# Performance work log

Measured on AMD Instinct MI355X. Metric: run time of the kernel, lower is better.

The kernel has to match this reference:

```python
import jax, jax.numpy as jnp
import numpy as np

BATCH, L, DM, DS, K, EXPAND = 4, 2048, 1024, 16, 4, 2
DI = EXPAND * DM  # 2048


def setup_inputs() -> dict:
    key = jax.random.key(0)
    ks = jax.random.split(key, 12)
    s = 0.02  # small init so exp(exp(dt)*A) and tanh stay well-behaved
    return {
        "x": jax.random.normal(ks[0], (BATCH, L, DM), jnp.float32),
        "W_in": jax.random.normal(ks[1], (2 * DI, DM), jnp.float32) * s,
        "b_in": jax.random.normal(ks[2], (2 * DI,), jnp.float32) * s,
        "conv_w": jax.random.normal(ks[3], (DI, 1, K), jnp.float32) * s,  # depthwise
        "conv_b": jax.random.normal(ks[4], (DI,), jnp.float32) * s,
        "W_x": jax.random.normal(ks[5], (2 * DS, DI), jnp.float32) * s,
        "b_x": jax.random.normal(ks[6], (2 * DS,), jnp.float32) * s,
        "dt": jax.random.normal(ks[7], (DI,), jnp.float32) * s,
        "A": jax.random.normal(ks[8], (DS, DS), jnp.float32) * s,
        "D": jnp.ones((DI,), jnp.float32),
        "W_out": jax.random.normal(ks[9], (DM, DI), jnp.float32) * s,
        "b_out": jax.random.normal(ks[10], (DM,), jnp.float32) * s,
    }


def _forward(x, W_in, b_in, conv_w, conv_b, W_x, b_x, dt, A, D, W_out, b_out):
    # in_proj: (B, L, 2*DI), split into conv path and residual
    xr = x @ W_in.T + b_in
    xi, res = jnp.split(xr, 2, axis=-1)
    # depthwise causal conv1d: torch pads both sides by K-1 then truncates to L,
    # equivalent to left-pad-only causal conv
    xc = jax.lax.conv_general_dilated(
        xi.transpose(0, 2, 1), conv_w, window_strides=(1,),
        padding=((K - 1, 0),), feature_group_count=DI,
        dimension_numbers=("NCH", "OIH", "NCH"))
    xc = (xc + conv_b[None, :, None]).transpose(0, 2, 1)  # (B, L, DI)
    xs = jax.nn.silu(xc)
    # x_proj -> B, C (each (B, L, DS))
    bc = xs @ W_x.T + b_x
    Bm, Cm = jnp.split(bc, 2, axis=-1)
    # dt = exp(self.dt) sliced to first DS entries, indexed per step by i % DS
    dtv = jnp.exp(dt)[:DS]
    dt_seq = dtv[jnp.arange(L) % DS]  # (L,)
    # NOTE: torch code computes x * D inside _selective_scan but never uses it;
    # the scan output depends only on dt, A, B, C.

    def step(h, inp):
        d_i, B_t, C_t = inp  # scalar, (B, DS), (B, DS)
        A_t = jnp.exp(d_i * A)  # (DS, DS)
        h_new = jnp.tanh(jnp.einsum("ij,bj->bi", A_t, h) + B_t * h + C_t)
        return h_new, h_new

    h0 = jnp.zeros((x.shape[0], DS), x.dtype)
    _, hs = jax.lax.scan(step, h0, (dt_seq, Bm.transpose(1, 0, 2), Cm.transpose(1, 0, 2)))
    hs = hs.transpose(1, 0, 2)  # (B, L, DS)
    y = jnp.tile(hs, (1, 1, DI // DS)) + res  # repeat state to d_inner, add res
    return y @ W_out.T + b_out


def reference(x, W_in, b_in, conv_w, conv_b, W_x, b_x, dt, A, D, W_out, b_out):
    return _forward(x, W_in, b_in, conv_w, conv_b, W_x, b_x, dt, A, D, W_out, b_out)
```

## Files before the change

### kernel.cpp

```cpp
#include <hip/hip_runtime.h>
#include <cstdint>
#include <cstddef>

typedef __attribute__((ext_vector_type(4))) float f32x4;
typedef __attribute__((ext_vector_type(8))) __bf16 bf16x8;
typedef __attribute__((ext_vector_type(4))) unsigned int u32x4;
typedef __attribute__((ext_vector_type(2))) unsigned int u32x2;

#define DEVFN static __device__ __forceinline__

#define OFF_XBF    0ull
#define OFF_WINBF  16777216ull
#define OFF_WXBF   25165824ull
#define OFF_WOUTBF 25296896ull
#define OFF_WRED   29491200ull
#define OFF_XIBF   29556736ull
#define OFF_RESBF  63111168ull
#define OFF_XSBF   96665600ull
#define OFF_BC     130220032ull
#define OFF_HS     131268608ull

DEVFN unsigned short f2bf(float f) {
  unsigned u = __float_as_uint(f);
  return (unsigned short)((u + 0x7FFFu + ((u >> 16) & 1u)) >> 16);
}

DEVFN void gload_lds16(const void* g, void* l) {
  __builtin_amdgcn_global_load_lds(
      (const __attribute__((address_space(1))) void*)g,
      (__attribute__((address_space(3))) void*)l, 16, 0, 0);
}

#define DPPF(x, ctrl) \
  __int_as_float(__builtin_amdgcn_update_dpp(0, __float_as_int(x), ctrl, 0xF, 0xF, true))

DEVFN void cvt8(const float* __restrict__ in, unsigned short* __restrict__ out, int t) {
  f32x4 a = *(const f32x4*)(in + (size_t)t * 8);
  f32x4 b = *(const f32x4*)(in + (size_t)t * 8 + 4);
  u32x4 r;
  r.x = (unsigned)f2bf(a[0]) | ((unsigned)f2bf(a[1]) << 16);
  r.y = (unsigned)f2bf(a[2]) | ((unsigned)f2bf(a[3]) << 16);
  r.z = (unsigned)f2bf(b[0]) | ((unsigned)f2bf(b[1]) << 16);
  r.w = (unsigned)f2bf(b[2]) | ((unsigned)f2bf(b[3]) << 16);
  *(u32x4*)(out + (size_t)t * 8) = r;
}

__global__ __launch_bounds__(256) void k_prep(
    const float* __restrict__ x, const float* __restrict__ W_in,
    const float* __restrict__ W_x, const float* __restrict__ W_out,
    unsigned short* __restrict__ xbf, unsigned short* __restrict__ winbf,
    unsigned short* __restrict__ wxbf, unsigned short* __restrict__ woutbf,
    float* __restrict__ wred) {
  const int bid = blockIdx.x, tid = threadIdx.x;
  if (bid < 4096)      cvt8(x,     xbf,    bid * 256 + tid);
  else if (bid < 6144) cvt8(W_in,  winbf,  (bid - 4096) * 256 + tid);
  else if (bid < 6176) cvt8(W_x,   wxbf,   (bid - 6144) * 256 + tid);
  else if (bid < 7200) cvt8(W_out, woutbf, (bid - 6176) * 256 + tid);
  else {
    const int t = (bid - 7200) * 256 + tid;
    const int m = t >> 4, j = t & 15;
    float s = 0.f;
    for (int r = 0; r < 128; r++) s += W_out[(size_t)m * 2048 + r * 16 + j];
    wred[t] = s;
  }
}

template <int EPI>
DEVFN void gemm128(const unsigned short* __restrict__ Ag,
                   const unsigned short* __restrict__ Bg, int K,
                   int m0, int n0, const float* __restrict__ bias,
                   float* __restrict__ outf,
                   unsigned short* __restrict__ ob0,
                   unsigned short* __restrict__ ob1) {
  __shared__ unsigned short As[128 * 64];
  __shared__ unsigned short Bs[128 * 64];
  const int tid = threadIdx.x;
  const int wave = tid >> 6, lane = tid & 63;
  const int wm = wave >> 1, wn = wave & 1;
  const int fr = lane & 15;
  const int k8 = (lane >> 4) << 3;

  f32x4 acc[4][4];
#pragma unroll
  for (int a = 0; a < 4; a++)
#pragma unroll
    for (int b = 0; b < 4; b++) acc[a][b] = f32x4{0.f, 0.f, 0.f, 0.f};

  for (int kt = 0; kt < K; kt += 64) {
#pragma unroll
    for (int i = 0; i < 4; i++) {
      const int base = (wave << 10) + (i << 12);
      const int off = base + (lane << 4);
      const int row = off >> 7;
      const int col = (off & 127) >> 1;
      gload_lds16(Ag + (size_t)(m0 + row) * K + kt + col, (char*)As + base);
      gload_lds16(Bg + (size_t)(n0 + row) * K + kt + col, (char*)Bs + base);
    }
    __syncthreads();
#pragma unroll
    for (int kk = 0; kk < 2; kk++) {
      bf16x8 af[4], bfr[4];
#pragma unroll
      for (int f = 0; f < 4; f++) {
        af[f]  = *(const bf16x8*)&As[(wm * 64 + f * 16 + fr) * 64 + kk * 32 + k8];
        bfr[f] = *(const bf16x8*)&Bs[(wn * 64 + f * 16 + fr) * 64 + kk * 32 + k8];
      }
#pragma unroll
      for (int fi = 0; fi < 4; fi++)
#pragma unroll
        for (int fj = 0; fj < 4; fj++)
          acc[fi][fj] = __builtin_amdgcn_mfma_f32_16x16x32_bf16(
              af[fi], bfr[fj], acc[fi][fj], 0, 0, 0);
    }
    __syncthreads();
  }

  const int r0 = (lane >> 4) * 4;
#pragma unroll
  for (int fj = 0; fj < 4; fj++) {
    const int col = n0 + wn * 64 + fj * 16 + fr;
    const float bia = (EPI == 0) ? bias[col] : 0.f;
#pragma unroll
    for (int fi = 0; fi < 4; fi++) {
      const int rowb = m0 + wm * 64 + fi * 16 + r0;
#pragma unroll
      for (int r = 0; r < 4; r++) {
        const float v = acc[fi][fj][r] + bia;
        if (EPI == 0) {
          if (col < 2048) ob0[(size_t)(rowb + r) * 2048 + col] = f2bf(v);
          else            ob1[(size_t)(rowb + r) * 2048 + (col - 2048)] = f2bf(v);
        } else {
          outf[(size_t)(rowb + r) * 1024 + col] = v;
        }
      }
    }
  }
}

__global__ __launch_bounds__(256) void k_gemm1(const unsigned short* __restrict__ xbf,
                                               const unsigned short* __restrict__ winbf,
                                               const float* __restrict__ b_in,
                                               unsigned short* __restrict__ xibf,
                                               unsigned short* __restrict__ resbf) {
  const int bid = blockIdx.x;
  gemm128<0>(xbf, winbf, 1024, (bid >> 5) * 128, (bid & 31) * 128, b_in,
             nullptr, xibf, resbf);
}

__global__ __launch_bounds__(256) void k_conv(const unsigned short* __restrict__ xi,
                                              const float* __restrict__ cw,
                                              const float* __restrict__ cb,
                                              unsigned short* __restrict__ xs) {
  const int t = blockIdx.x * 256 + threadIdx.x;
  const int c4 = t & 511;
  const int lc = (t >> 9) & 255;
  const int b  = t >> 17;
  const int l0 = lc * 8;
  const int c0 = c4 * 4;
  const unsigned short* xb = xi + ((size_t)(b * 2048 + l0)) * 2048 + c0;
  u32x2 raw[11];
#pragma unroll
  for (int j = 0; j < 11; j++) {
    const int l = l0 + j - 3;
    raw[j] = (l >= 0) ? *(const u32x2*)(xb + ((long)j - 3) * 2048) : u32x2{0u, 0u};
  }
  f32x4 val[11];
#pragma unroll
  for (int j = 0; j < 11; j++) {
    val[j][0] = __uint_as_float(raw[j].x << 16);
    val[j][1] = __uint_as_float(raw[j].x & 0xFFFF0000u);
    val[j][2] = __uint_as_float(raw[j].y << 16);
    val[j][3] = __uint_as_float(raw[j].y & 0xFFFF0000u);
  }
  const f32x4 w0 = *(const f32x4*)(cw + (size_t)c0 * 4);
  const f32x4 w1 = *(const f32x4*)(cw + (size_t)(c0 + 1) * 4);
  const f32x4 w2 = *(const f32x4*)(cw + (size_t)(c0 + 2) * 4);
  const f32x4 w3 = *(const f32x4*)(cw + (size_t)(c0 + 3) * 4);
  const f32x4 bb = *(const f32x4*)(cb + c0);
  unsigned short* xp = xs + ((size_t)(b * 2048 + l0)) * 2048 + c0;
#pragma unroll
  for (int jo = 0; jo < 8; jo++) {
    f32x4 v;
    v[0] = bb[0] + w0[0]*val[jo][0] + w0[1]*val[jo+1][0] + w0[2]*val[jo+2][0] + w0[3]*val[jo+3][0];
    v[1] = bb[1] + w1[0]*val[jo][1] + w1[1]*val[jo+1][1] + w1[2]*val[jo+2][1] + w1[3]*val[jo+3][1];
    v[2] = bb[2] + w2[0]*val[jo][2] + w2[1]*val[jo+1][2] + w2[2]*val[jo+2][2] + w2[3]*val[jo+3][2];
    v[3] = bb[3] + w3[0]*val[jo][3] + w3[1]*val[jo+1][3] + w3[2]*val[jo+2][3] + w3[3]*val[jo+3][3];
#pragma unroll
    for (int q = 0; q < 4; q++) {
      const float x = v[q];
      v[q] = x * __builtin_amdgcn_rcpf(1.f + __expf(-x));
    }
    u32x2 rr;
    rr.x = (unsigned)f2bf(v[0]) | ((unsigned)f2bf(v[1]) << 16);
    rr.y = (unsigned)f2bf(v[2]) | ((unsigned)f2bf(v[3]) << 16);
    *(u32x2*)(xp + (size_t)jo * 2048) = rr;
  }
}

__global__ __launch_bounds__(256) void k_gemm2(const unsigned short* __restrict__ xs,
                                               const unsigned short* __restrict__ wx,
                                               const float* __restrict__ bx,
                                               float* __restrict__ bc) {
  __shared__ unsigned short As[128 * 64];
  __shared__ unsigned short Bs[32 * 64];
  const int tid = threadIdx.x, wave = tid >> 6, lane = tid & 63;
  const int m0 = blockIdx.x * 128;
  const int fr = lane & 15, k8 = (lane >> 4) << 3;
  f32x4 acc[2][2];
#pragma unroll
  for (int a = 0; a < 2; a++)
#pragma unroll
    for (int b = 0; b < 2; b++) acc[a][b] = f32x4{0.f, 0.f, 0.f, 0.f};

  for (int kt = 0; kt < 2048; kt += 64) {
#pragma unroll
    for (int i = 0; i < 4; i++) {
      const int base = (wave << 10) + (i << 12);
      const int off = base + (lane << 4);
      const int row = off >> 7, col = (off & 127) >> 1;
      gload_lds16(xs + (size_t)(m0 + row) * 2048 + kt + col, (char*)As + base);
    }
    {
      const int base = (wave << 10);
      const int off = base + (lane << 4);
      const int row = off >> 7, col = (off & 127) >> 1;
      gload_lds16(wx + (size_t)row * 2048 + kt + col, (char*)Bs + base);
    }
    __syncthreads();
#pragma unroll
    for (int kk = 0; kk < 2; kk++) {
      bf16x8 af[2], bfr[2];
#pragma unroll
      for (int f = 0; f < 2; f++) {
        af[f]  = *(const bf16x8*)&As[(wave * 32 + f * 16 + fr) * 64 + kk * 32 + k8];
        bfr[f] = *(const bf16x8*)&Bs[(f * 16 + fr) * 64 + kk * 32 + k8];
      }
#pragma unroll
      for (int fi = 0; fi < 2; fi++)
#pragma unroll
        for (int fj = 0; fj < 2; fj++)
          acc[fi][fj] = __builtin_amdgcn_mfma_f32_16x16x32_bf16(
              af[fi], bfr[fj], acc[fi][fj], 0, 0, 0);
    }
    __syncthreads();
  }
  const int r0 = (lane >> 4) * 4;
#pragma unroll
  for (int fi = 0; fi < 2; fi++)
#pragma unroll
    for (int fj = 0; fj < 2; fj++) {
      const int col = fj * 16 + fr;
      const float bia = bx[col];
#pragma unroll
      for (int r = 0; r < 4; r++) {
        const int row = m0 + wave * 32 + fi * 16 + r0 + r;
        bc[(size_t)row * 32 + col] = acc[fi][fj][r] + bia;
      }
    }
}

DEVFN float scan4_step(float h, const f32x4 ax, float Bt, float Ct, int a0) {
  const int hv = __float_as_int(h);
  const float g0 = __int_as_float(__builtin_amdgcn_ds_bpermute(a0,      hv));
  const float g1 = __int_as_float(__builtin_amdgcn_ds_bpermute(a0 + 16, hv));
  const float g2 = __int_as_float(__builtin_amdgcn_ds_bpermute(a0 + 32, hv));
  const float g3 = __int_as_float(__builtin_amdgcn_ds_bpermute(a0 + 48, hv));
  const float pa = fmaf(ax[1], g1, ax[0] * g0);
  const float pb = fmaf(ax[3], g3, ax[2] * g2);
  float p = pa + pb;
  p += DPPF(p, 0xB1);
  p += DPPF(p, 0x4E);
  const float s = p + fmaf(Bt, h, Ct);
  const float e = __expf(2.f * s);
  return fmaf(-2.f, __builtin_amdgcn_rcpf(e + 1.f), 1.f);
}

__global__ __launch_bounds__(256) void k4_gemm3_scan(
    const unsigned short* __restrict__ resbf, const unsigned short* __restrict__ woutbf,
    float* __restrict__ out, const float* __restrict__ bc, const float* __restrict__ dt,
    const float* __restrict__ Amat, float* __restrict__ hs) {
  if (blockIdx.x < 512) {
    const int bid = blockIdx.x;
    gemm128<1>(resbf, woutbf, 2048, (bid >> 3) * 128, (bid & 7) * 128, nullptr,
               out, nullptr, nullptr);
    return;
  }
  const int tid = threadIdx.x;
  const int b = tid >> 6;
  const int lane = tid & 63;
  const int i = lane >> 2, k = lane & 3;

  const f32x4 arow = *(const f32x4*)(Amat + i * 16 + k * 4);
  f32x4 axv[16];
#pragma unroll
  for (int p = 0; p < 16; p++) {
    const float e = __expf(dt[p]);
    axv[p][0] = __expf(e * arow[0]);
    axv[p][1] = __expf(e * arow[1]);
    axv[p][2] = __expf(e * arow[2]);
    axv[p][3] = __expf(e * arow[3]);
  }
  const int a0 = (lane & 3) << 6;
  const float* bcp = bc + (size_t)b * 65536 + i;
  float* hsp = hs + (size_t)b * 32768 + i;
  float h = 0.f;

  float p0B[8], p0C[8], p1B[8], p1C[8];
#pragma unroll
  for (int q = 0; q < 8; q++) { p0B[q] = bcp[q * 32]; p0C[q] = bcp[q * 32 + 16]; }

  for (int l0 = 0; l0 < 2048; l0 += 16) {
    {
      const float* bq = bcp + (size_t)(l0 + 8) * 32;
#pragma unroll
      for (int q = 0; q < 8; q++) { p1B[q] = bq[q * 32]; p1C[q] = bq[q * 32 + 16]; }
    }
#pragma unroll
    for (int q = 0; q < 8; q++) {
      h = scan4_step(h, axv[q], p0B[q], p0C[q], a0);
      if (k == 0) hsp[(size_t)(l0 + q) * 16] = h;
    }
    {
      const float* bq = bcp + (size_t)((l0 + 16) & 2047) * 32;
#pragma unroll
      for (int q = 0; q < 8; q++) { p0B[q] = bq[q * 32]; p0C[q] = bq[q * 32 + 16]; }
    }
#pragma unroll
    for (int q = 8; q < 16; q++) {
      h = scan4_step(h, axv[q], p1B[q - 8], p1C[q - 8], a0);
      if (k == 0) hsp[(size_t)(l0 + q) * 16] = h;
    }
  }
}

__global__ __launch_bounds__(256) void k5_combine(float* __restrict__ out,
                                                  const float* __restrict__ hs,
                                                  const float* __restrict__ wred,
                                                  const float* __restrict__ bo) {
  const int m4 = threadIdx.x;
  const int rg = blockIdx.x;
  f32x4 w[4][4];
#pragma unroll
  for (int mi = 0; mi < 4; mi++)
#pragma unroll
    for (int q = 0; q < 4; q++)
      w[mi][q] = *(const f32x4*)&wred[(size_t)(m4 * 4 + mi) * 16 + q * 4];
  const f32x4 bov = *(const f32x4*)&bo[m4 * 4];
#pragma unroll
  for (int r = 0; r < 4; r++) {
    const size_t row = (size_t)rg * 4 + r;
    f32x4 hv[4];
#pragma unroll
    for (int q = 0; q < 4; q++) hv[q] = *(const f32x4*)&hs[row * 16 + q * 4];
    float* op = out + row * 1024 + m4 * 4;
    f32x4 o = *(f32x4*)op;
#pragma unroll
    for (int mi = 0; mi < 4; mi++) {
      float v = bov[mi];
#pragma unroll
      for (int q = 0; q < 4; q++)
        v += w[mi][q][0]*hv[q][0] + w[mi][q][1]*hv[q][1] +
             w[mi][q][2]*hv[q][2] + w[mi][q][3]*hv[q][3];
      o[mi] += v;
    }
    *(f32x4*)op = o;
  }
}

extern "C" void kernel_launch(void* const* d_in, const int* in_sizes, int n_in,
                              void* d_out, int out_size, void* d_ws, size_t ws_size,
                              hipStream_t stream) {
  const float* x      = (const float*)d_in[0];
  const float* W_in   = (const float*)d_in[1];
  const float* b_in   = (const float*)d_in[2];
  const float* conv_w = (const float*)d_in[3];
  const float* conv_b = (const float*)d_in[4];
  const float* W_x    = (const float*)d_in[5];
  const float* b_x    = (const float*)d_in[6];
  const float* dt     = (const float*)d_in[7];
  const float* A      = (const float*)d_in[8];
  const float* W_out  = (const float*)d_in[10];
  const float* b_out  = (const float*)d_in[11];
  float* out = (float*)d_out;

  char* ws = (char*)d_ws;
  unsigned short* xbf    = (unsigned short*)(ws + OFF_XBF);
  unsigned short* winbf  = (unsigned short*)(ws + OFF_WINBF);
  unsigned short* wxbf   = (unsigned short*)(ws + OFF_WXBF);
  unsigned short* woutbf = (unsigned short*)(ws + OFF_WOUTBF);
  float*          wred   = (float*)(ws + OFF_WRED);
  unsigned short* xibf   = (unsigned short*)(ws + OFF_XIBF);
  unsigned short* resbf  = (unsigned short*)(ws + OFF_RESBF);
  unsigned short* xsbf   = (unsigned short*)(ws + OFF_XSBF);
  float*          bc     = (float*)(ws + OFF_BC);
  float*          hsb    = (float*)(ws + OFF_HS);

  k_prep<<<7264, 256, 0, stream>>>(x, W_in, W_x, W_out, xbf, winbf, wxbf, woutbf, wred);
  k_gemm1<<<2048, 256, 0, stream>>>(xbf, winbf, b_in, xibf, resbf);
  k_conv<<<2048, 256, 0, stream>>>(xibf, conv_w, conv_b, xsbf);
  k_gemm2<<<64, 256, 0, stream>>>(xsbf, wxbf, b_x, bc);
  k4_gemm3_scan<<<513, 256, 0, stream>>>(resbf, woutbf, out, bc, dt, A, hsb);
  k5_combine<<<2048, 256, 0, stream>>>(out, hsb, wred, b_out);
}
```

Before: 516.8 us.

## Replace LDS bpermute gathers in recurrent scan with DPP row rotates and permlane swaps

The serial 16-state recurrence is remapped so lane P of each 16-lane row holds state P, and each of the four rows handles a different column quarter of A. The per-step state gather moves from four ds_bpermute LDS round-trips to DPP row rotates, and the cross-row sum uses permlane16/32 swaps. The B/C term is pre-scaled by 0.25 so the four-way reduction sums it only once. This targets the latency of the serial critical path, which bounds the scan part of the kernel, at the cost of more intricate lane indexing and the risk of mis-mapped A columns.

```diff
diff --git a/kernel.cpp b/kernel.cpp
--- a/kernel.cpp
+++ b/kernel.cpp
@@ -33,6 +33,8 @@
 
 #define DPPF(x, ctrl) \
   __int_as_float(__builtin_amdgcn_update_dpp(0, __float_as_int(x), ctrl, 0xF, 0xF, true))
+#define DPPI(x, ctrl) \
+  __builtin_amdgcn_update_dpp(0, (x), ctrl, 0xF, 0xF, true)
 
 DEVFN void cvt8(const float* __restrict__ in, unsigned short* __restrict__ out, int t) {
   f32x4 a = *(const f32x4*)(in + (size_t)t * 8);
@@ -259,20 +261,32 @@
     }
 }
 
-DEVFN float scan4_step(float h, const f32x4 ax, float Bt, float Ct, int a0) {
-  const int hv = __float_as_int(h);
-  const float g0 = __int_as_float(__builtin_amdgcn_ds_bpermute(a0,      hv));
-  const float g1 = __int_as_float(__builtin_amdgcn_ds_bpermute(a0 + 16, hv));
-  const float g2 = __int_as_float(__builtin_amdgcn_ds_bpermute(a0 + 32, hv));
-  const float g3 = __int_as_float(__builtin_amdgcn_ds_bpermute(a0 + 48, hv));
-  const float pa = fmaf(ax[1], g1, ax[0] * g0);
-  const float pb = fmaf(ax[3], g3, ax[2] * g2);
-  float p = pa + pb;
-  p += DPPF(p, 0xB1);
-  p += DPPF(p, 0x4E);
-  const float s = p + fmaf(Bt, h, Ct);
-  const float e = __expf(2.f * s);
-  return fmaf(-2.f, __builtin_amdgcn_rcpf(e + 1.f), 1.f);
+DEVFN float scan_step_dpp(float h, const f32x4 ax, float bq, float cq,
+                          bool modd, bool m23) {
+  const float bcterm = fmaf(bq, h, cq);
+  const float r1 = DPPF(h, 0x121);
+  const float t  = modd ? r1 : h;
+  const float r2 = DPPF(t, 0x122);
+  const float X  = m23 ? r2 : t;
+  const float V1 = DPPF(X, 0x124);
+  const float V2 = DPPF(X, 0x128);
+  const float V3 = DPPF(X, 0x12C);
+  float p01 = fmaf(ax[0], X, bcterm);
+  p01 = fmaf(ax[1], V1, p01);
+  float p23 = ax[2] * V2;
+  p23 = fmaf(ax[3], V3, p23);
+  float p = p01 + p23;
+  {
+    u32x2 r16 = __builtin_amdgcn_permlane16_swap(
+        __float_as_uint(p), __float_as_uint(p), false, false);
+    p = __uint_as_float(r16[0]) + __uint_as_float(r16[1]);
+    u32x2 r32 = __builtin_amdgcn_permlane32_swap(
+        __float_as_uint(p), __float_as_uint(p), false, false);
+    p = __uint_as_float(r32[0]) + __uint_as_float(r32[1]);
+  }
+  const float e = exp2f(p * 2.8853900817779268f);
+  const float u = __builtin_amdgcn_rcpf(e + 1.f);
+  return fmaf(-2.f, u, 1.f);
 }
 
 __global__ __launch_bounds__(256) void k4_gemm3_scan(
@@ -288,47 +302,61 @@
   const int tid = threadIdx.x;
   const int b = tid >> 6;
   const int lane = tid & 63;
-  const int i = lane >> 2, k = lane & 3;
-
-  const f32x4 arow = *(const f32x4*)(Amat + i * 16 + k * 4);
+  const int P = lane & 15, R = lane >> 4;
+  const bool modd = (R & 1) != 0, m23 = (R & 2) != 0;
+
+  int pr1 = DPPI(P, 0x121); int pt = modd ? pr1 : P;
+  int pr2 = DPPI(pt, 0x122); int pX = m23 ? pr2 : pt;
+  const int c0 = pX;
+  const int c1 = DPPI(pX, 0x124);
+  const int c2 = DPPI(pX, 0x128);
+  const int c3 = DPPI(pX, 0x12C);
+
+  const float a0 = Amat[P * 16 + c0], a1 = Amat[P * 16 + c1];
+  const float a2 = Amat[P * 16 + c2], a3 = Amat[P * 16 + c3];
   f32x4 axv[16];
 #pragma unroll
   for (int p = 0; p < 16; p++) {
     const float e = __expf(dt[p]);
-    axv[p][0] = __expf(e * arow[0]);
-    axv[p][1] = __expf(e * arow[1]);
-    axv[p][2] = __expf(e * arow[2]);
-    axv[p][3] = __expf(e * arow[3]);
-  }
-  const int a0 = (lane & 3) << 6;
-  const float* bcp = bc + (size_t)b * 65536 + i;
-  float* hsp = hs + (size_t)b * 32768 + i;
+    axv[p][0] = __expf(e * a0);
+    axv[p][1] = __expf(e * a1);
+    axv[p][2] = __expf(e * a2);
+    axv[p][3] = __expf(e * a3);
+  }
+  const float* bcp = bc + (size_t)b * 65536 + P;
+  float* hsp = hs + (size_t)b * 32768 + P;
   float h = 0.f;
 
   float p0B[8], p0C[8], p1B[8], p1C[8];
 #pragma unroll
-  for (int q = 0; q < 8; q++) { p0B[q] = bcp[q * 32]; p0C[q] = bcp[q * 32 + 16]; }
+  for (int q = 0; q < 8; q++) {
+    p0B[q] = bcp[q * 32] * 0.25f; p0C[q] = bcp[q * 32 + 16] * 0.25f;
+  }
 
   for (int l0 = 0; l0 < 2048; l0 += 16) {
     {
       const float* bq = bcp + (size_t)(l0 + 8) * 32;
 #pragma unroll
-      for (int q = 0; q < 8; q++) { p1B[q] = bq[q * 32]; p1C[q] = bq[q * 32 + 16]; }
+      for (int q = 0; q < 8; q++) {
+        p1B[q] = bq[q * 32] * 0.25f; p1C[q] = bq[q * 32 + 16] * 0.25f;
+      }
     }
 #pragma unroll
     for (int q = 0; q < 8; q++) {
-      h = scan4_step(h, axv[q], p0B[q], p0C[q], a0);
-      if (k == 0) hsp[(size_t)(l0 + q) * 16] = h;
+      h = scan_step_dpp(h, axv[q], p0B[q], p0C[q], modd, m23);
+      if (R == 0) hsp[(size_t)(l0 + q) * 16] = h;
     }
     {
       const float* bq = bcp + (size_t)((l0 + 16) & 2047) * 32;
 #pragma unroll
-      for (int q = 0; q < 8; q++) { p0B[q] = bq[q * 32]; p0C[q] = bq[q * 32 + 16]; }
+      for (int q = 0; q < 8; q++) {
+        p0B[q] = bq[q * 32] * 0.25f; p0C[q] = bq[q * 32 + 16] * 0.25f;
+      }
     }
 #pragma unroll
     for (int q = 8; q < 16; q++) {
-      h = scan4_step(h, axv[q], p1B[q - 8], p1C[q - 8], a0);
-      if (k == 0) hsp[(size_t)(l0 + q) * 16] = h;
+      h = scan_step_dpp(h, axv[q], p1B[q - 8], p1C[q - 8], modd, m23);
+      if (R == 0) hsp[(size_t)(l0 + q) * 16] = h;
     }
   }
 }
```

Result: slower. 531.5 us (+2.8%).

## Fold residual projection into output GEMM via precomputed combined weight

Applied to the files above, without the earlier changes.

The residual branch is linear, so the code now precomputes Wc = W_out · W_in_res with a small GEMM each call. It also folds W_out·b_res + b_out into a constant bias. The in-projection GEMM now only produces the conv half (N=2048 instead of 4096). The output GEMM multiplies x directly by Wc with K=1024 instead of reading a bf16 res tensor with K=2048. This removes a large share of the GEMM FLOPs and the res intermediate traffic. In exchange it adds a transpose in prep and an extra under-filled 64-block kernel, and rounds the combined weight to bf16.

```diff
diff --git a/kernel.cpp b/kernel.cpp
--- a/kernel.cpp
+++ b/kernel.cpp
@@ -11,14 +11,16 @@
 
 #define OFF_XBF    0ull
 #define OFF_WINBF  16777216ull
-#define OFF_WXBF   25165824ull
-#define OFF_WOUTBF 25296896ull
-#define OFF_WRED   29491200ull
-#define OFF_XIBF   29556736ull
-#define OFF_RESBF  63111168ull
-#define OFF_XSBF   96665600ull
-#define OFF_BC     130220032ull
-#define OFF_HS     131268608ull
+#define OFF_WXBF   20971520ull
+#define OFF_WOUTBF 21102592ull
+#define OFF_WRT    25296896ull
+#define OFF_WC     29491200ull
+#define OFF_WRED   31588352ull
+#define OFF_BCONST 31653888ull
+#define OFF_XIBF   31657984ull
+#define OFF_XSBF   65212416ull
+#define OFF_BC     98766848ull
+#define OFF_HS     99815424ull
 
 DEVFN unsigned short f2bf(float f) {
   unsigned u = __float_as_uint(f);
@@ -48,20 +50,59 @@
 __global__ __launch_bounds__(256) void k_prep(
     const float* __restrict__ x, const float* __restrict__ W_in,
     const float* __restrict__ W_x, const float* __restrict__ W_out,
+    const float* __restrict__ b_in, const float* __restrict__ b_out,
     unsigned short* __restrict__ xbf, unsigned short* __restrict__ winbf,
     unsigned short* __restrict__ wxbf, unsigned short* __restrict__ woutbf,
-    float* __restrict__ wred) {
+    unsigned short* __restrict__ wrtbf, float* __restrict__ wred,
+    float* __restrict__ bconst) {
   const int bid = blockIdx.x, tid = threadIdx.x;
-  if (bid < 4096)      cvt8(x,     xbf,    bid * 256 + tid);
-  else if (bid < 6144) cvt8(W_in,  winbf,  (bid - 4096) * 256 + tid);
-  else if (bid < 6176) cvt8(W_x,   wxbf,   (bid - 6144) * 256 + tid);
-  else if (bid < 7200) cvt8(W_out, woutbf, (bid - 6176) * 256 + tid);
-  else {
-    const int t = (bid - 7200) * 256 + tid;
+  if (bid < 4096)      { cvt8(x,     xbf,    bid * 256 + tid); return; }
+  if (bid < 5120)      { cvt8(W_in,  winbf,  (bid - 4096) * 256 + tid); return; }
+  if (bid < 5152)      { cvt8(W_x,   wxbf,   (bid - 5120) * 256 + tid); return; }
+  if (bid < 6176)      { cvt8(W_out, woutbf, (bid - 5152) * 256 + tid); return; }
+  if (bid < 6240) {
+    const int t = (bid - 6176) * 256 + tid;
     const int m = t >> 4, j = t & 15;
     float s = 0.f;
     for (int r = 0; r < 128; r++) s += W_out[(size_t)m * 2048 + r * 16 + j];
     wred[t] = s;
+    return;
+  }
+  if (bid < 6256) {
+    const int t = (bid - 6240) * 256 + tid;
+    const int m = t >> 2, q = t & 3;
+    const float* wr = W_out + (size_t)m * 2048 + q * 512;
+    const float* bi = b_in + 2048 + q * 512;
+    float s = 0.f;
+    for (int j = 0; j < 128; j++) {
+      const f32x4 w = *(const f32x4*)(wr + j * 4);
+      const f32x4 v = *(const f32x4*)(bi + j * 4);
+      s += w[0]*v[0] + w[1]*v[1] + w[2]*v[2] + w[3]*v[3];
+    }
+    s += DPPF(s, 0xB1);
+    s += DPPF(s, 0x4E);
+    if ((tid & 3) == 0) bconst[m] = b_out[m] + s;
+    return;
+  }
+  __shared__ float lt[64][65];
+  const int tt = bid - 6256;
+  const int d0 = (tt >> 4) * 64, k0 = (tt & 15) * 64;
+  const int r16 = tid >> 4, c4 = tid & 15;
+#pragma unroll
+  for (int i = 0; i < 4; i++) {
+    const int dr = r16 + i * 16;
+    const f32x4 v = *(const f32x4*)(W_in + (size_t)(2048 + d0 + dr) * 1024 + k0 + c4 * 4);
+    lt[dr][c4 * 4 + 0] = v[0]; lt[dr][c4 * 4 + 1] = v[1];
+    lt[dr][c4 * 4 + 2] = v[2]; lt[dr][c4 * 4 + 3] = v[3];
+  }
+  __syncthreads();
+#pragma unroll
+  for (int i = 0; i < 4; i++) {
+    const int kr = r16 + i * 16;
+    u32x2 rr;
+    rr.x = (unsigned)f2bf(lt[c4 * 4 + 0][kr]) | ((unsigned)f2bf(lt[c4 * 4 + 1][kr]) << 16);
+    rr.y = (unsigned)f2bf(lt[c4 * 4 + 2][kr]) | ((unsigned)f2bf(lt[c4 * 4 + 3][kr]) << 16);
+    *(u32x2*)(wrtbf + (size_t)(k0 + kr) * 2048 + d0 + c4 * 4) = rr;
   }
 }
 
@@ -69,9 +110,7 @@
 DEVFN void gemm128(const unsigned short* __restrict__ Ag,
                    const unsigned short* __restrict__ Bg, int K,
                    int m0, int n0, const float* __restrict__ bias,
-                   float* __restrict__ outf,
-                   unsigned short* __restrict__ ob0,
-                   unsigned short* __restrict__ ob1) {
+                   float* __restrict__ outf, unsigned short* __restrict__ outbf) {
   __shared__ unsigned short As[128 * 64];
   __shared__ unsigned short Bs[128 * 64];
   const int tid = threadIdx.x;
@@ -119,32 +158,35 @@
 #pragma unroll
   for (int fj = 0; fj < 4; fj++) {
     const int col = n0 + wn * 64 + fj * 16 + fr;
-    const float bia = (EPI == 0) ? bias[col] : 0.f;
+    const float bia = (EPI == 2) ? 0.f : bias[col];
 #pragma unroll
     for (int fi = 0; fi < 4; fi++) {
       const int rowb = m0 + wm * 64 + fi * 16 + r0;
 #pragma unroll
       for (int r = 0; r < 4; r++) {
         const float v = acc[fi][fj][r] + bia;
-        if (EPI == 0) {
-          if (col < 2048) ob0[(size_t)(rowb + r) * 2048 + col] = f2bf(v);
-          else            ob1[(size_t)(rowb + r) * 2048 + (col - 2048)] = f2bf(v);
-        } else {
-          outf[(size_t)(rowb + r) * 1024 + col] = v;
-        }
+        if (EPI == 0)      outbf[(size_t)(rowb + r) * 2048 + col] = f2bf(v);
+        else if (EPI == 1) outf[(size_t)(rowb + r) * 1024 + col] = v;
+        else               outbf[(size_t)(rowb + r) * 1024 + col] = f2bf(v);
       }
     }
   }
+}
+
+__global__ __launch_bounds__(256) void k_wc(const unsigned short* __restrict__ woutbf,
+                                            const unsigned short* __restrict__ wrtbf,
+                                            unsigned short* __restrict__ wcbf) {
+  const int bid = blockIdx.x;
+  gemm128<2>(woutbf, wrtbf, 2048, (bid >> 3) * 128, (bid & 7) * 128, nullptr,
+             nullptr, wcbf);
 }
 
 __global__ __launch_bounds__(256) void k_gemm1(const unsigned short* __restrict__ xbf,
                                                const unsigned short* __restrict__ winbf,
                                                const float* __restrict__ b_in,
-                                               unsigned short* __restrict__ xibf,
-                                               unsigned short* __restrict__ resbf) {
+                                               unsigned short* __restrict__ xibf) {
   const int bid = blockIdx.x;
-  gemm128<0>(xbf, winbf, 1024, (bid >> 5) * 128, (bid & 31) * 128, b_in,
-             nullptr, xibf, resbf);
+  gemm128<0>(xbf, winbf, 1024, (bid >> 4) * 128, (bid & 15) * 128, b_in, nullptr, xibf);
 }
 
 __global__ __launch_bounds__(256) void k_conv(const unsigned short* __restrict__ xi,
@@ -275,14 +317,15 @@
   return fmaf(-2.f, __builtin_amdgcn_rcpf(e + 1.f), 1.f);
 }
 
-__global__ __launch_bounds__(256) void k4_gemm3_scan(
-    const unsigned short* __restrict__ resbf, const unsigned short* __restrict__ woutbf,
-    float* __restrict__ out, const float* __restrict__ bc, const float* __restrict__ dt,
+__global__ __launch_bounds__(256) void k4_gemm_scan(
+    const unsigned short* __restrict__ xbf, const unsigned short* __restrict__ wcbf,
+    const float* __restrict__ bconst, float* __restrict__ out,
+    const float* __restrict__ bc, const float* __restrict__ dt,
     const float* __restrict__ Amat, float* __restrict__ hs) {
   if (blockIdx.x < 512) {
     const int bid = blockIdx.x;
-    gemm128<1>(resbf, woutbf, 2048, (bid >> 3) * 128, (bid & 7) * 128, nullptr,
-               out, nullptr, nullptr);
+    gemm128<1>(xbf, wcbf, 1024, (bid >> 3) * 128, (bid & 7) * 128, bconst,
+               out, nullptr);
     return;
   }
   const int tid = threadIdx.x;
@@ -335,8 +378,7 @@
 
 __global__ __launch_bounds__(256) void k5_combine(float* __restrict__ out,
                                                   const float* __restrict__ hs,
-                                                  const float* __restrict__ wred,
-                                                  const float* __restrict__ bo) {
+                                                  const float* __restrict__ wred) {
   const int m4 = threadIdx.x;
   const int rg = blockIdx.x;
   f32x4 w[4][4];
@@ -345,7 +387,6 @@
 #pragma unroll
     for (int q = 0; q < 4; q++)
       w[mi][q] = *(const f32x4*)&wred[(size_t)(m4 * 4 + mi) * 16 + q * 4];
-  const f32x4 bov = *(const f32x4*)&bo[m4 * 4];
 #pragma unroll
   for (int r = 0; r < 4; r++) {
     const size_t row = (size_t)rg * 4 + r;
@@ -356,7 +397,7 @@
     f32x4 o = *(f32x4*)op;
 #pragma unroll
     for (int mi = 0; mi < 4; mi++) {
-      float v = bov[mi];
+      float v = 0.f;
 #pragma unroll
       for (int q = 0; q < 4; q++)
         v += w[mi][q][0]*hv[q][0] + w[mi][q][1]*hv[q][1] +
@@ -388,17 +429,21 @@
   unsigned short* winbf  = (unsigned short*)(ws + OFF_WINBF);
   unsigned short* wxbf   = (unsigned short*)(ws + OFF_WXBF);
   unsigned short* woutbf = (unsigned short*)(ws + OFF_WOUTBF);
+  unsigned short* wrtbf  = (unsigned short*)(ws + OFF_WRT);
+  unsigned short* wcbf   = (unsigned short*)(ws + OFF_WC);
   float*          wred   = (float*)(ws + OFF_WRED);
+  float*          bconst = (float*)(ws + OFF_BCONST);
   unsigned short* xibf   = (unsigned short*)(ws + OFF_XIBF);
-  unsigned short* resbf  = (unsigned short*)(ws + OFF_RESBF);
   unsigned short* xsbf   = (unsigned short*)(ws + OFF_XSBF);
   float*          bc     = (float*)(ws + OFF_BC);
   float*          hsb    = (float*)(ws + OFF_HS);
 
-  k_prep<<<7264, 256, 0, stream>>>(x, W_in, W_x, W_out, xbf, winbf, wxbf, woutbf, wred);
-  k_gemm1<<<2048, 256, 0, stream>>>(xbf, winbf, b_in, xibf, resbf);
+  k_prep<<<6768, 256, 0, stream>>>(x, W_in, W_x, W_out, b_in, b_out,
+                                   xbf, winbf, wxbf, woutbf, wrtbf, wred, bconst);
+  k_wc<<<64, 256, 0, stream>>>(woutbf, wrtbf, wcbf);
+  k_gemm1<<<1024, 256, 0, stream>>>(xbf, winbf, b_in, xibf);
   k_conv<<<2048, 256, 0, stream>>>(xibf, conv_w, conv_b, xsbf);
   k_gemm2<<<64, 256, 0, stream>>>(xsbf, wxbf, b_x, bc);
-  k4_gemm3_scan<<<513, 256, 0, stream>>>(resbf, woutbf, out, bc, dt, A, hsb);
-  k5_combine<<<2048, 256, 0, stream>>>(out, hsb, wred, b_out);
-}
+  k4_gemm_scan<<<513, 256, 0, stream>>>(xbf, wcbf, bconst, out, bc, dt, A, hsb);
+  k5_combine<<<2048, 256, 0, stream>>>(out, hsb, wred);
+}
```

Result: no change. 508.4 us (-1.6%).
